# Optimization experiments

Hardware: AMD Instinct MI355X
Metric: run time of the kernel (lower is better)

The kernel has to match this reference:

```python
import jax, jax.numpy as jnp
import numpy as np

N_NODES = 20000
N_EDGES = 320000
DIMS = [256, 256, 128, 64]  # input_dim, hidden_dims...
EPS = 1e-5


def gcn_conv(x, w, b, src, dst, n):
    # PyG GCNConv: linear first, then symmetric-normalized aggregation with self-loops
    x = x @ w  # [N, out]
    loops = jnp.arange(n, dtype=src.dtype)
    src2 = jnp.concatenate([src, loops])
    dst2 = jnp.concatenate([dst, loops])
    deg = jax.ops.segment_sum(jnp.ones_like(dst2, dtype=x.dtype), dst2, num_segments=n)
    dinv = jnp.where(deg > 0, deg ** -0.5, 0.0)
    norm = dinv[src2] * dinv[dst2]  # [E+N]
    msg = x[src2] * norm[:, None]   # gathered, scaled messages
    out = jax.ops.segment_sum(msg, dst2, num_segments=n)
    return out + b


def graph_norm(x, w, b, a):
    # PyG GraphNorm over a single graph: per-feature mean/var across nodes
    mean = jnp.mean(x, axis=0)
    centered = x - a * mean
    var = jnp.mean(centered * centered, axis=0)
    return w * centered * jax.lax.rsqrt(var + EPS) + b


def layer_norm(x, w, b):
    mean = jnp.mean(x, axis=-1, keepdims=True)
    var = jnp.mean((x - mean) ** 2, axis=-1, keepdims=True)
    return (x - mean) * jax.lax.rsqrt(var + EPS) * w + b


def setup_inputs() -> dict:
    key = jax.random.key(0)
    ks = jax.random.split(key, 32)
    inp = {}
    inp["x"] = jax.random.normal(ks[0], (N_NODES, DIMS[0]), dtype=jnp.float32)
    inp["edge_index"] = jax.random.randint(ks[1], (2, N_EDGES), 0, N_NODES, dtype=jnp.int32)
    ki = 2
    for i in range(3):
        fin, fout = DIMS[i], DIMS[i + 1]
        s = 1.0 / np.sqrt(fin)
        inp[f"w{i}"] = jax.random.uniform(ks[ki], (fin, fout), jnp.float32, -s, s); ki += 1
        inp[f"b{i}"] = jnp.zeros((fout,), jnp.float32)
        inp[f"gn{i}_w"] = jnp.ones((fout,), jnp.float32)
        inp[f"gn{i}_b"] = jnp.zeros((fout,), jnp.float32)
        inp[f"gn{i}_a"] = jnp.ones((fout,), jnp.float32)
    h = DIMS[-1]
    s = 1.0 / np.sqrt(3 * h)
    inp["wc1"] = jax.random.uniform(ks[ki], (3 * h, h), jnp.float32, -s, s); ki += 1
    inp["bc1"] = jnp.zeros((h,), jnp.float32)
    inp["ln_w"] = jnp.ones((h,), jnp.float32)
    inp["ln_b"] = jnp.zeros((h,), jnp.float32)
    s = 1.0 / np.sqrt(h)
    inp["wc2"] = jax.random.uniform(ks[ki], (h, 2), jnp.float32, -s, s); ki += 1
    inp["bc2"] = jnp.zeros((2,), jnp.float32)
    return inp


def reference(x, edge_index,
              w0, b0, gn0_w, gn0_b, gn0_a,
              w1, b1, gn1_w, gn1_b, gn1_a,
              w2, b2, gn2_w, gn2_b, gn2_a,
              wc1, bc1, ln_w, ln_b, wc2, bc2):
    src, dst = edge_index[0], edge_index[1]
    n = x.shape[0]
    params = [(w0, b0, gn0_w, gn0_b, gn0_a),
              (w1, b1, gn1_w, gn1_b, gn1_a),
              (w2, b2, gn2_w, gn2_b, gn2_a)]
    for (w, b, gw, gb, ga) in params:
        x_res = x
        x = gcn_conv(x, w, b, src, dst, n)
        x = graph_norm(x, gw, gb, ga)
        x = jax.nn.gelu(x, approximate=False)
        # dropout = identity (eval); residual only when shapes match (layer 0)
        if x.shape == x_res.shape:
            x = x + x_res
    # multi-pool over the single graph (batch vector of zeros): mean | max | sum
    pooled = jnp.concatenate([jnp.mean(x, axis=0), jnp.max(x, axis=0), jnp.sum(x, axis=0)])[None, :]  # [1, 3h]
    h = pooled @ wc1 + bc1
    h = layer_norm(h, ln_w, ln_b)
    h = jax.nn.gelu(h, approximate=False)
    return h @ wc2 + bc2  # [1, num_classes]
```

## Files before the change

### kernel.cpp

```cpp
#include <hip/hip_runtime.h>
#include <math.h>

#define EPSV 1e-5f
#define MAXB 2176
#define GBLK 2080

typedef __attribute__((ext_vector_type(8))) short short8;
typedef __attribute__((ext_vector_type(4))) float f32x4;

__device__ __forceinline__ float gelu_f(float x) {
    return 0.5f * x * (1.0f + erff(x * 0.70710678118654752440f));
}

__device__ __forceinline__ float4 f4add(float4 a, float4 b) {
    return make_float4(a.x + b.x, a.y + b.y, a.z + b.z, a.w + b.w);
}

__device__ __forceinline__ ushort f2bf(float v) {
    union { float f; unsigned u; } a; a.f = v;
    unsigned r = a.u + 0x7FFFu + ((a.u >> 16) & 1u);
    return (ushort)(r >> 16);
}
__device__ __forceinline__ float bf2f(ushort h) {
    union { unsigned u; float f; } a; a.u = ((unsigned)h) << 16;
    return a.f;
}
__device__ __forceinline__ float4 bf4f(ushort4 v) {
    return make_float4(bf2f(v.x), bf2f(v.y), bf2f(v.z), bf2f(v.w));
}

__global__ void deg_kernel(const int* __restrict__ ei, int* __restrict__ deg, int E) {
    int stride = gridDim.x * blockDim.x;
    for (int e = blockIdx.x * blockDim.x + threadIdx.x; e < E; e += stride)
        atomicAdd(&deg[ei[E + e]], 1);
}

__global__ __launch_bounds__(1024) void scan_kernel(const int* __restrict__ deg,
                                                    int* __restrict__ off,
                                                    float* __restrict__ dinv, int N) {
    __shared__ int sh[1024];
    int t = threadIdx.x;
    int chunk = (N + 1023) >> 10;
    int b = t * chunk;
    int e = b + chunk; if (e > N) e = N;
    int s = 0;
    for (int i = b; i < e; ++i) s += deg[i];
    sh[t] = s;
    __syncthreads();
    for (int d = 1; d < 1024; d <<= 1) {
        int v = (t >= d) ? sh[t - d] : 0;
        __syncthreads();
        sh[t] += v;
        __syncthreads();
    }
    int run = (t > 0) ? sh[t - 1] : 0;
    for (int i = b; i < e; ++i) {
        off[i] = run;
        run += deg[i];
        dinv[i] = rsqrtf((float)(deg[i] + 1));
    }
    if (t == 1023) off[N] = sh[1023];
}

__global__ void fill_kernel(const int* __restrict__ ei, const int* __restrict__ off,
                            int* __restrict__ fill, int* __restrict__ csr, int E) {
    int stride = gridDim.x * blockDim.x;
    for (int e = blockIdx.x * blockDim.x + threadIdx.x; e < E; e += stride) {
        int d = ei[E + e];
        int p = off[d] + atomicAdd(&fill[d], 1);
        csr[p] = ei[e];
    }
}

__global__ __launch_bounds__(256) void packx_kernel(
    const float* __restrict__ x, ushort* __restrict__ hi, ushort* __restrict__ lo, long n)
{
    long stride = (long)gridDim.x * blockDim.x * 4;
    for (long i = ((long)blockIdx.x * blockDim.x + threadIdx.x) * 4; i < n; i += stride) {
        float4 v = *(const float4*)(x + i);
        ushort4 h, l2;
        h.x = f2bf(v.x); h.y = f2bf(v.y); h.z = f2bf(v.z); h.w = f2bf(v.w);
        l2.x = f2bf(v.x - bf2f(h.x)); l2.y = f2bf(v.y - bf2f(h.y));
        l2.z = f2bf(v.z - bf2f(h.z)); l2.w = f2bf(v.w - bf2f(h.w));
        *(ushort4*)(hi + i) = h;
        *(ushort4*)(lo + i) = l2;
    }
}

__global__ void packw_all_kernel(const float* __restrict__ w0, const float* __restrict__ w1,
                                 const float* __restrict__ w2,
                                 ushort* __restrict__ wthi, ushort* __restrict__ wtlo)
{
    int idx = blockIdx.x * 256 + threadIdx.x;
    const float* W; int K, F, base, local;
    if (idx < 65536)       { W = w0; K = 256; F = 256; base = 0;     local = idx; }
    else if (idx < 98304)  { W = w1; K = 256; F = 128; base = 65536; local = idx - 65536; }
    else if (idx < 106496) { W = w2; K = 128; F = 64;  base = 98304; local = idx - 98304; }
    else return;
    int k = local / F, f = local - k * F;
    float v = W[local];
    ushort h = f2bf(v);
    wthi[base + f * K + k] = h;
    wtlo[base + f * K + k] = f2bf(v - bf2f(h));
}

template<int K, int BN>
__global__ __launch_bounds__(256) void gemm_mfma_kernel(
    const ushort* __restrict__ ahi, const ushort* __restrict__ alo,
    const ushort* __restrict__ wthi, const ushort* __restrict__ wtlo,
    const float* __restrict__ dinv, ushort* __restrict__ C,
    int M, int F)
{
    constexpr int BM = 128, BK = 64;
    constexpr int LDK = BK + 8;
    constexpr int CF  = BN / 32;
    constexpr int WCH = BN / 32;

    __shared__ ushort AsH[BM * LDK], AsL[BM * LDK];
    __shared__ ushort WsH[BN * LDK], WsL[BN * LDK];

    const int tid = threadIdx.x;
    const int l = tid & 63, w = tid >> 6;
    const int wr = w >> 1, wc = w & 1;
    const int m0   = blockIdx.y * BM;
    const int colB = blockIdx.x * BN;
    const int lr = l & 15, lkg = l >> 4;

    f32x4 acc[4][CF] = {};

    for (int kk = 0; kk < K; kk += BK) {
        short8 ra[4], rb[4], rwh[WCH], rwl[WCH];
#pragma unroll
        for (int i = 0; i < 4; ++i) {
            int q = tid + i * 256;
            int row = q >> 3, cc = q & 7;
            int rg = m0 + row; if (rg > M - 1) rg = M - 1;
            ra[i] = *(const short8*)(ahi + (size_t)rg * K + kk + cc * 8);
            rb[i] = *(const short8*)(alo + (size_t)rg * K + kk + cc * 8);
        }
#pragma unroll
        for (int i = 0; i < WCH; ++i) {
            int q = tid + i * 256;
            int row = q >> 3, cc = q & 7;
            rwh[i] = *(const short8*)(wthi + (size_t)(colB + row) * K + kk + cc * 8);
            rwl[i] = *(const short8*)(wtlo + (size_t)(colB + row) * K + kk + cc * 8);
        }
        __syncthreads();
#pragma unroll
        for (int i = 0; i < 4; ++i) {
            int q = tid + i * 256;
            int row = q >> 3, cc = q & 7;
            *(short8*)&AsH[row * LDK + cc * 8] = ra[i];
            *(short8*)&AsL[row * LDK + cc * 8] = rb[i];
        }
#pragma unroll
        for (int i = 0; i < WCH; ++i) {
            int q = tid + i * 256;
            int row = q >> 3, cc = q & 7;
            *(short8*)&WsH[row * LDK + cc * 8] = rwh[i];
            *(short8*)&WsL[row * LDK + cc * 8] = rwl[i];
        }
        __syncthreads();

#pragma unroll
        for (int ks = 0; ks < 2; ++ks) {
            const int kof = ks * 32 + lkg * 8;
            short8 afh[4], afl[4];
#pragma unroll
            for (int rf = 0; rf < 4; ++rf) {
                int row = wr * 64 + rf * 16 + lr;
                afh[rf] = *(const short8*)&AsH[row * LDK + kof];
                afl[rf] = *(const short8*)&AsL[row * LDK + kof];
            }
            short8 wfh[CF], wfl[CF];
#pragma unroll
            for (int cf = 0; cf < CF; ++cf) {
                int row = wc * (BN / 2) + cf * 16 + lr;
                wfh[cf] = *(const short8*)&WsH[row * LDK + kof];
                wfl[cf] = *(const short8*)&WsL[row * LDK + kof];
            }
#pragma unroll
            for (int rf = 0; rf < 4; ++rf) {
#pragma unroll
                for (int cf = 0; cf < CF; ++cf) {
                    acc[rf][cf] = __builtin_amdgcn_mfma_f32_16x16x32_bf16(afh[rf], wfh[cf], acc[rf][cf], 0, 0, 0);
                    acc[rf][cf] = __builtin_amdgcn_mfma_f32_16x16x32_bf16(afh[rf], wfl[cf], acc[rf][cf], 0, 0, 0);
                    acc[rf][cf] = __builtin_amdgcn_mfma_f32_16x16x32_bf16(afl[rf], wfh[cf], acc[rf][cf], 0, 0, 0);
                }
            }
        }
    }

#pragma unroll
    for (int rf = 0; rf < 4; ++rf) {
#pragma unroll
        for (int j = 0; j < 4; ++j) {
            int r = m0 + wr * 64 + rf * 16 + lkg * 4 + j;
            if (r < M) {
                float dv = dinv[r];
                ushort* Cp = C + (size_t)r * F + colB + wc * (BN / 2) + lr;
#pragma unroll
                for (int cf = 0; cf < CF; ++cf)
                    Cp[cf * 16] = f2bf(acc[rf][cf][j] * dv);
            }
        }
    }
}

template<int F>
__global__ __launch_bounds__(256) void gather_kernel(
    const ushort* __restrict__ hs, const int* __restrict__ off,
    const int* __restrict__ csr, const float* __restrict__ dinv,
    const float* __restrict__ bias, float* __restrict__ t,
    float* __restrict__ p1, float* __restrict__ p2, int N)
{
    constexpr int NG  = F / 64;
    constexpr int LDR = F / 4;
    constexpr int NPB = 16;
    const int lane = threadIdx.x & 15;
    const int slot = threadIdx.x >> 4;

    const int xs    = blockIdx.x & 7;
    const int g     = xs % NG;
    const int r     = xs / NG;
    const int chunk = blockIdx.x >> 3;
    const int repl  = 8 / NG;
    const int nPerG = (int)(gridDim.x >> 3) * repl;
    const int j     = chunk * repl + r;

    const int col4 = g * 16 + lane;
    const int c0 = col4 * 4;
    float4* t4 = (float4*)t;
    const float4 bv = ((const float4*)bias)[col4];

    float4 a1 = make_float4(0.f, 0.f, 0.f, 0.f);
    float4 a2 = make_float4(0.f, 0.f, 0.f, 0.f);

    for (int d = j * NPB + slot; d < N; d += nPerG * NPB) {
        float4 acc = bf4f(*(const ushort4*)(hs + (size_t)d * F + c0));
        const int e0 = off[d], e1 = off[d + 1];
        int e = e0;
        for (; e + 8 <= e1; e += 8) {
            int s0 = csr[e + 0], s1 = csr[e + 1], s2 = csr[e + 2], s3 = csr[e + 3];
            int s4 = csr[e + 4], s5 = csr[e + 5], s6 = csr[e + 6], s7 = csr[e + 7];
            ushort4 v0 = *(const ushort4*)(hs + (size_t)s0 * F + c0);
            ushort4 v1 = *(const ushort4*)(hs + (size_t)s1 * F + c0);
            ushort4 v2 = *(const ushort4*)(hs + (size_t)s2 * F + c0);
            ushort4 v3 = *(const ushort4*)(hs + (size_t)s3 * F + c0);
            ushort4 v4 = *(const ushort4*)(hs + (size_t)s4 * F + c0);
            ushort4 v5 = *(const ushort4*)(hs + (size_t)s5 * F + c0);
            ushort4 v6 = *(const ushort4*)(hs + (size_t)s6 * F + c0);
            ushort4 v7 = *(const ushort4*)(hs + (size_t)s7 * F + c0);
            float4 u0 = f4add(bf4f(v0), bf4f(v1));
            float4 u1 = f4add(bf4f(v2), bf4f(v3));
            float4 u2 = f4add(bf4f(v4), bf4f(v5));
            float4 u3 = f4add(bf4f(v6), bf4f(v7));
            acc = f4add(acc, f4add(f4add(u0, u1), f4add(u2, u3)));
        }
        for (; e + 2 <= e1; e += 2) {
            int s0 = csr[e + 0], s1 = csr[e + 1];
            ushort4 v0 = *(const ushort4*)(hs + (size_t)s0 * F + c0);
            ushort4 v1 = *(const ushort4*)(hs + (size_t)s1 * F + c0);
            acc = f4add(acc, f4add(bf4f(v0), bf4f(v1)));
        }
        if (e < e1) {
            acc = f4add(acc, bf4f(*(const ushort4*)(hs + (size_t)csr[e] * F + c0)));
        }

        float dv = dinv[d];
        float4 o;
        o.x = fmaf(dv, acc.x, bv.x);
        o.y = fmaf(dv, acc.y, bv.y);
        o.z = fmaf(dv, acc.z, bv.z);
        o.w = fmaf(dv, acc.w, bv.w);
        t4[(long)d * LDR + col4] = o;
        a1.x += o.x; a1.y += o.y; a1.z += o.z; a1.w += o.w;
        a2.x += o.x * o.x; a2.y += o.y * o.y; a2.z += o.z * o.z; a2.w += o.w * o.w;
    }

    __shared__ float red[8][256];
    red[0][threadIdx.x] = a1.x; red[1][threadIdx.x] = a1.y;
    red[2][threadIdx.x] = a1.z; red[3][threadIdx.x] = a1.w;
    red[4][threadIdx.x] = a2.x; red[5][threadIdx.x] = a2.y;
    red[6][threadIdx.x] = a2.z; red[7][threadIdx.x] = a2.w;
    __syncthreads();
    if (slot == 0) {
        float sum[8];
#pragma unroll
        for (int k = 0; k < 8; ++k) {
            float s = red[k][lane];
            for (int jj = 1; jj < NPB; ++jj) s += red[k][jj * 16 + lane];
            sum[k] = s;
        }
        ((float4*)p1)[(long)col4 * MAXB + blockIdx.x] = make_float4(sum[0], sum[1], sum[2], sum[3]);
        ((float4*)p2)[(long)col4 * MAXB + blockIdx.x] = make_float4(sum[4], sum[5], sum[6], sum[7]);
    }
}

__global__ __launch_bounds__(256) void statreduce_kernel(
    const float* __restrict__ p1, const float* __restrict__ p2,
    const float* __restrict__ ga,
    float* __restrict__ meanv, float* __restrict__ istdv,
    int nb, int N, int NG)
{
    const int c4 = blockIdx.x;
    const int g = (c4 >> 4) % NG;
    const float4* p14 = (const float4*)p1 + (long)c4 * MAXB;
    const float4* p24 = (const float4*)p2 + (long)c4 * MAXB;
    float4 a1 = make_float4(0.f, 0.f, 0.f, 0.f);
    float4 a2 = make_float4(0.f, 0.f, 0.f, 0.f);
    for (int r = threadIdx.x; r < nb; r += 256) {
        if (((r & 7) % NG) != g) continue;
        float4 v1 = p14[r];
        float4 v2 = p24[r];
        a1.x += v1.x; a1.y += v1.y; a1.z += v1.z; a1.w += v1.w;
        a2.x += v2.x; a2.y += v2.y; a2.z += v2.z; a2.w += v2.w;
    }
#pragma unroll
    for (int offv = 32; offv > 0; offv >>= 1) {
        a1.x += __shfl_down(a1.x, offv); a1.y += __shfl_down(a1.y, offv);
        a1.z += __shfl_down(a1.z, offv); a1.w += __shfl_down(a1.w, offv);
        a2.x += __shfl_down(a2.x, offv); a2.y += __shfl_down(a2.y, offv);
        a2.z += __shfl_down(a2.z, offv); a2.w += __shfl_down(a2.w, offv);
    }
    __shared__ float4 sh1[4], sh2[4];
    const int wid = threadIdx.x >> 6;
    if ((threadIdx.x & 63) == 0) { sh1[wid] = a1; sh2[wid] = a2; }
    __syncthreads();
    if (threadIdx.x == 0) {
        float4 t1 = sh1[0], t2 = sh2[0];
        for (int jj = 1; jj < 4; ++jj) {
            float4 u1 = sh1[jj], u2 = sh2[jj];
            t1.x += u1.x; t1.y += u1.y; t1.z += u1.z; t1.w += u1.w;
            t2.x += u2.x; t2.y += u2.y; t2.z += u2.z; t2.w += u2.w;
        }
        float s1a[4] = { t1.x, t1.y, t1.z, t1.w };
        float s2a[4] = { t2.x, t2.y, t2.z, t2.w };
#pragma unroll
        for (int k = 0; k < 4; ++k) {
            int c = c4 * 4 + k;
            float m = s1a[k] / (float)N;
            float a = ga[c];
            float var = s2a[k] / (float)N - 2.f * a * m * m + a * a * m * m;
            meanv[c] = m;
            istdv[c] = rsqrtf(var + EPSV);
        }
    }
}

__global__ __launch_bounds__(256) void normgelu_kernel(
    const float* __restrict__ t, const float* __restrict__ meanv,
    const float* __restrict__ istdv, const float* __restrict__ gw,
    const float* __restrict__ gb, const float* __restrict__ ga,
    const float* __restrict__ res,
    ushort* __restrict__ ohi, ushort* __restrict__ olo,
    float* __restrict__ fpout,
    int log2f, long total)
{
    long stride = (long)gridDim.x * blockDim.x;
    int fmask = (1 << log2f) - 1;
    for (long idx = (long)blockIdx.x * blockDim.x + threadIdx.x; idx < total; idx += stride) {
        int c = (int)idx & fmask;
        float v = t[idx];
        float y = gw[c] * (v - ga[c] * meanv[c]) * istdv[c] + gb[c];
        y = gelu_f(y);
        if (res) y += res[idx];
        if (ohi) {
            ushort h = f2bf(y);
            ohi[idx] = h;
            olo[idx] = f2bf(y - bf2f(h));
        } else {
            fpout[idx] = y;
        }
    }
}

__device__ __forceinline__ void atomicMaxFloat(float* addr, float val) {
    unsigned* ua = (unsigned*)addr;
    unsigned old = *ua;
    while (true) {
        float of = __uint_as_float(old);
        if (of >= val) break;
        unsigned assumed = old;
        old = atomicCAS(ua, assumed, __float_as_uint(val));
        if (old == assumed) break;
    }
}

__global__ void initpool_kernel(float* __restrict__ psum, float* __restrict__ pmax) {
    int t = threadIdx.x;
    psum[t] = 0.f;
    pmax[t] = -INFINITY;
}

__global__ __launch_bounds__(256) void colpool_kernel(
    const float* __restrict__ x, float* __restrict__ psum, float* __restrict__ pmax,
    int M, int rowsPerBlock)
{
    int c = threadIdx.x & 63;
    int rl = threadIdx.x >> 6;
    int r0 = blockIdx.x * rowsPerBlock;
    int rend = r0 + rowsPerBlock; if (rend > M) rend = M;
    float a1 = 0.f, am = -INFINITY;
    for (int r = r0 + rl; r < rend; r += 4) {
        float v = x[(long)r * 64 + c];
        a1 += v; am = fmaxf(am, v);
    }
    __shared__ float sh1[256], shm[256];
    sh1[threadIdx.x] = a1; shm[threadIdx.x] = am;
    __syncthreads();
    if (threadIdx.x < 64) {
        for (int j = 1; j < 4; ++j) {
            a1 += sh1[c + j * 64];
            am = fmaxf(am, shm[c + j * 64]);
        }
        atomicAdd(&psum[c], a1);
        atomicMaxFloat(&pmax[c], am);
    }
}

__global__ void head_kernel(const float* __restrict__ psum, const float* __restrict__ pmax,
                            const float* __restrict__ wc1, const float* __restrict__ bc1,
                            const float* __restrict__ lnw, const float* __restrict__ lnb,
                            const float* __restrict__ wc2, const float* __restrict__ bc2,
                            float* __restrict__ out, int M)
{
    __shared__ float p[192];
    int t = threadIdx.x;
    float s = psum[t];
    p[t] = s / (float)M;
    p[64 + t] = pmax[t];
    p[128 + t] = s;
    __syncthreads();
    float h = bc1[t];
    for (int k = 0; k < 192; ++k) h = fmaf(p[k], wc1[k * 64 + t], h);
    float m = h;
    for (int off = 32; off > 0; off >>= 1) m += __shfl_xor(m, off);
    m *= (1.f / 64.f);
    float d = h - m;
    float v = d * d;
    for (int off = 32; off > 0; off >>= 1) v += __shfl_xor(v, off);
    v *= (1.f / 64.f);
    float y = d * rsqrtf(v + EPSV) * lnw[t] + lnb[t];
    y = gelu_f(y);
    float o0 = y * wc2[t * 2 + 0];
    float o1 = y * wc2[t * 2 + 1];
    for (int off = 32; off > 0; off >>= 1) {
        o0 += __shfl_xor(o0, off);
        o1 += __shfl_xor(o1, off);
    }
    if (t == 0) {
        out[0] = o0 + bc2[0];
        out[1] = o1 + bc2[1];
    }
}

extern "C" void kernel_launch(void* const* d_in, const int* in_sizes, int n_in,
                              void* d_out, int out_size, void* d_ws, size_t ws_size,
                              hipStream_t stream)
{
    const float* x    = (const float*)d_in[0];
    const int*   ei   = (const int*)d_in[1];
    const float* w0   = (const float*)d_in[2];
    const float* b0   = (const float*)d_in[3];
    const float* gn0w = (const float*)d_in[4];
    const float* gn0b = (const float*)d_in[5];
    const float* gn0a = (const float*)d_in[6];
    const float* w1   = (const float*)d_in[7];
    const float* b1   = (const float*)d_in[8];
    const float* gn1w = (const float*)d_in[9];
    const float* gn1b = (const float*)d_in[10];
    const float* gn1a = (const float*)d_in[11];
    const float* w2   = (const float*)d_in[12];
    const float* b2   = (const float*)d_in[13];
    const float* gn2w = (const float*)d_in[14];
    const float* gn2b = (const float*)d_in[15];
    const float* gn2a = (const float*)d_in[16];
    const float* wc1  = (const float*)d_in[17];
    const float* bc1  = (const float*)d_in[18];
    const float* lnw  = (const float*)d_in[19];
    const float* lnb  = (const float*)d_in[20];
    const float* wc2  = (const float*)d_in[21];
    const float* bc2  = (const float*)d_in[22];

    const int N = in_sizes[0] / 256;
    const int E = in_sizes[1] / 2;

    float* ws = (float*)d_ws;
    const size_t BIG = (size_t)N * 256;
    float* B0    = ws;
    float* B1    = ws + BIG;
    float* dinv  = ws + 2 * BIG;
    int*   deg   = (int*)(dinv + N);
    int*   fill  = deg + N;
    int*   off   = fill + N;
    int*   csr   = off + N + 1;
    float* p1    = (float*)(csr + E);
    float* p2    = p1 + (size_t)64 * MAXB * 4;
    float* meanv = p2 + (size_t)64 * MAXB * 4;
    float* istdv = meanv + 256;
    float* psum  = istdv + 256;
    float* pmax  = psum + 64;
    ushort* wthi = (ushort*)(pmax + 64);
    ushort* wtlo = wthi + 106496;
    const int woff[3] = { 0, 65536, 98304 };

    hipMemsetAsync(deg, 0, (size_t)2 * N * sizeof(int), stream);
    deg_kernel<<<1024, 256, 0, stream>>>(ei, deg, E);
    scan_kernel<<<1, 1024, 0, stream>>>(deg, off, dinv, N);
    fill_kernel<<<1024, 256, 0, stream>>>(ei, off, fill, csr, E);

    packw_all_kernel<<<416, 256, 0, stream>>>(w0, w1, w2, wthi, wtlo);
    packx_kernel<<<1280, 256, 0, stream>>>(x, (ushort*)B0, (ushort*)B0 + BIG, (long)BIG);

    struct Layer {
        const float *b, *gw, *gb, *ga;
        int K, F, lf;
    } L[3] = {
        { b0, gn0w, gn0b, gn0a, 256, 256, 8 },
        { b1, gn1w, gn1b, gn1a, 256, 128, 7 },
        { b2, gn2w, gn2b, gn2a, 128,  64, 6 },
    };
    const float* resb[3] = { x, nullptr, nullptr };
    float* Bb[2] = { B0, B1 };

    int cur = 0;
    for (int li = 0; li < 3; ++li) {
        const int K = L[li].K, F = L[li].F, lf = L[li].lf;
        const long total = (long)N << lf;
        float* Ab = Bb[cur];
        float* HSf = Bb[cur ^ 1];
        ushort* ahi = (ushort*)Ab;
        ushort* alo = ahi + BIG;
        ushort* HS = (ushort*)HSf;

        const int rowTiles = (N + 127) / 128;
        if (li == 0) {
            gemm_mfma_kernel<256, 128><<<dim3(2, rowTiles), 256, 0, stream>>>(
                ahi, alo, wthi + woff[0], wtlo + woff[0], dinv, HS, N, F);
        } else if (li == 1) {
            gemm_mfma_kernel<256, 128><<<dim3(1, rowTiles), 256, 0, stream>>>(
                ahi, alo, wthi + woff[1], wtlo + woff[1], dinv, HS, N, F);
        } else {
            gemm_mfma_kernel<128, 64><<<dim3(1, rowTiles), 256, 0, stream>>>(
                ahi, alo, wthi + woff[2], wtlo + woff[2], dinv, HS, N, F);
        }

        float* T = Ab;
        if (F == 256)
            gather_kernel<256><<<GBLK, 256, 0, stream>>>(HS, off, csr, dinv, L[li].b, T, p1, p2, N);
        else if (F == 128)
            gather_kernel<128><<<GBLK, 256, 0, stream>>>(HS, off, csr, dinv, L[li].b, T, p1, p2, N);
        else
            gather_kernel<64><<<GBLK, 256, 0, stream>>>(HS, off, csr, dinv, L[li].b, T, p1, p2, N);

        statreduce_kernel<<<F / 4, 256, 0, stream>>>(p1, p2, L[li].ga, meanv, istdv, GBLK, N, F / 64);

        long fb = (total + 255) / 256; if (fb > 4096) fb = 4096;
        ushort* ohi = (li < 2) ? (ushort*)HSf : nullptr;
        ushort* olo = (li < 2) ? (ushort*)HSf + BIG : nullptr;
        float*  fpo = (li == 2) ? HSf : nullptr;
        normgelu_kernel<<<(int)fb, 256, 0, stream>>>(T, meanv, istdv,
                                                     L[li].gw, L[li].gb, L[li].ga,
                                                     resb[li], ohi, olo, fpo, lf, total);
        cur ^= 1;
    }

    initpool_kernel<<<1, 64, 0, stream>>>(psum, pmax);
    colpool_kernel<<<(N + 127) / 128, 256, 0, stream>>>(Bb[cur], psum, pmax, N, 128);
    head_kernel<<<1, 64, 0, stream>>>(psum, pmax, wc1, bc1, lnw, lnb, wc2, bc2,
                                      (float*)d_out, N);
}
```

Measured before the change: 280.0 us.

## Fuse small kernels via last-block reductions and convert input inside GEMM

Folds the degree scan into the degree-count kernel, the per-feature stat reduction into the gather kernel, and pooling plus the classifier head into one kernel. Each uses an atomic counter so the last finishing block does the final reduction. The separate pass that splits x into bf16 hi/lo is removed, and the layer-0 GEMM now does that split on the fp32 input as it loads it. The norm+GELU kernel is vectorised to float4. This cuts kernel launches and one full pass over x, but the final reductions now run on a single block, which serialises that step.

Result: slower. 1.060 ms (+278.6%).

```diff
diff --git a/kernel.cpp b/kernel.cpp
--- a/kernel.cpp
+++ b/kernel.cpp
@@ -28,26 +28,44 @@
 __device__ __forceinline__ float4 bf4f(ushort4 v) {
     return make_float4(bf2f(v.x), bf2f(v.y), bf2f(v.z), bf2f(v.w));
 }
-
-__global__ void deg_kernel(const int* __restrict__ ei, int* __restrict__ deg, int E) {
+__device__ __forceinline__ void f8_to_bf(const float4 f0, const float4 f1,
+                                         short8& h, short8& l) {
+    union { short8 v; ushort u[8]; } H, L;
+    float f[8] = { f0.x, f0.y, f0.z, f0.w, f1.x, f1.y, f1.z, f1.w };
+#pragma unroll
+    for (int j = 0; j < 8; ++j) {
+        H.u[j] = f2bf(f[j]);
+        L.u[j] = f2bf(f[j] - bf2f(H.u[j]));
+    }
+    h = H.v; l = L.v;
+}
+
+__global__ __launch_bounds__(256) void deg_scan_kernel(
+    const int* __restrict__ ei, int* __restrict__ deg,
+    int* __restrict__ off, float* __restrict__ dinv,
+    int E, int N, int* __restrict__ ctr)
+{
     int stride = gridDim.x * blockDim.x;
     for (int e = blockIdx.x * blockDim.x + threadIdx.x; e < E; e += stride)
         atomicAdd(&deg[ei[E + e]], 1);
-}
-
-__global__ __launch_bounds__(1024) void scan_kernel(const int* __restrict__ deg,
-                                                    int* __restrict__ off,
-                                                    float* __restrict__ dinv, int N) {
-    __shared__ int sh[1024];
-    int t = threadIdx.x;
-    int chunk = (N + 1023) >> 10;
+    __threadfence();
+    __shared__ int lastBlk;
+    if (threadIdx.x == 0)
+        lastBlk = (atomicAdd(ctr, 1) == (int)gridDim.x - 1);
+    __syncthreads();
+    if (!lastBlk) return;
+    __threadfence();
+
+    __shared__ int sh[256];
+    const int t = threadIdx.x;
+    const int chunk = (N + 255) >> 8;
     int b = t * chunk;
     int e = b + chunk; if (e > N) e = N;
     int s = 0;
     for (int i = b; i < e; ++i) s += deg[i];
     sh[t] = s;
     __syncthreads();
-    for (int d = 1; d < 1024; d <<= 1) {
+    for (int d = 1; d < 256; d <<= 1) {
         int v = (t >= d) ? sh[t - d] : 0;
         __syncthreads();
         sh[t] += v;
@@ -55,11 +73,12 @@
     }
     int run = (t > 0) ? sh[t - 1] : 0;
     for (int i = b; i < e; ++i) {
+        int dg = deg[i];
         off[i] = run;
-        run += deg[i];
-        dinv[i] = rsqrtf((float)(deg[i] + 1));
-    }
-    if (t == 1023) off[N] = sh[1023];
+        dinv[i] = rsqrtf((float)(dg + 1));
+        run += dg;
+    }
+    if (t == 255) off[N] = sh[255];
 }
 
 __global__ void fill_kernel(const int* __restrict__ ei, const int* __restrict__ off,
@@ -69,21 +88,6 @@
         int d = ei[E + e];
         int p = off[d] + atomicAdd(&fill[d], 1);
         csr[p] = ei[e];
-    }
-}
-
-__global__ __launch_bounds__(256) void packx_kernel(
-    const float* __restrict__ x, ushort* __restrict__ hi, ushort* __restrict__ lo, long n)
-{
-    long stride = (long)gridDim.x * blockDim.x * 4;
-    for (long i = ((long)blockIdx.x * blockDim.x + threadIdx.x) * 4; i < n; i += stride) {
-        float4 v = *(const float4*)(x + i);
-        ushort4 h, l2;
-        h.x = f2bf(v.x); h.y = f2bf(v.y); h.z = f2bf(v.z); h.w = f2bf(v.w);
-        l2.x = f2bf(v.x - bf2f(h.x)); l2.y = f2bf(v.y - bf2f(h.y));
-        l2.z = f2bf(v.z - bf2f(h.z)); l2.w = f2bf(v.w - bf2f(h.w));
-        *(ushort4*)(hi + i) = h;
-        *(ushort4*)(lo + i) = l2;
     }
 }
 
@@ -104,9 +108,10 @@
     wtlo[base + f * K + k] = f2bf(v - bf2f(h));
 }
 
-template<int K, int BN>
+template<int K, int BN, bool AF32>
 __global__ __launch_bounds__(256) void gemm_mfma_kernel(
     const ushort* __restrict__ ahi, const ushort* __restrict__ alo,
+    const float* __restrict__ axf,
     const ushort* __restrict__ wthi, const ushort* __restrict__ wtlo,
     const float* __restrict__ dinv, ushort* __restrict__ C,
     int M, int F)
@@ -135,8 +140,13 @@
             int q = tid + i * 256;
             int row = q >> 3, cc = q & 7;
             int rg = m0 + row; if (rg > M - 1) rg = M - 1;
-            ra[i] = *(const short8*)(ahi + (size_t)rg * K + kk + cc * 8);
-            rb[i] = *(const short8*)(alo + (size_t)rg * K + kk + cc * 8);
+            if constexpr (AF32) {
+                const float* xp = axf + (size_t)rg * K + kk + cc * 8;
+                f8_to_bf(*(const float4*)xp, *(const float4*)(xp + 4), ra[i], rb[i]);
+            } else {
+                ra[i] = *(const short8*)(ahi + (size_t)rg * K + kk + cc * 8);
+                rb[i] = *(const short8*)(alo + (size_t)rg * K + kk + cc * 8);
+            }
         }
 #pragma unroll
         for (int i = 0; i < WCH; ++i) {
@@ -212,7 +222,10 @@
     const ushort* __restrict__ hs, const int* __restrict__ off,
     const int* __restrict__ csr, const float* __restrict__ dinv,
     const float* __restrict__ bias, float* __restrict__ t,
-    float* __restrict__ p1, float* __restrict__ p2, int N)
+    float* __restrict__ p1, float* __restrict__ p2,
+    const float* __restrict__ ga,
+    float* __restrict__ meanv, float* __restrict__ istdv,
+    int N, int* __restrict__ ctr)
 {
     constexpr int NG  = F / 64;
     constexpr int LDR = F / 4;
@@ -288,57 +301,53 @@
         float sum[8];
 #pragma unroll
         for (int k = 0; k < 8; ++k) {
-            float s = red[k][lane];
-            for (int jj = 1; jj < NPB; ++jj) s += red[k][jj * 16 + lane];
+            float s = red[k][threadIdx.x];
+            for (int jj = 1; jj < NPB; ++jj) s += red[k][jj * 16 + threadIdx.x];
             sum[k] = s;
         }
         ((float4*)p1)[(long)col4 * MAXB + blockIdx.x] = make_float4(sum[0], sum[1], sum[2], sum[3]);
         ((float4*)p2)[(long)col4 * MAXB + blockIdx.x] = make_float4(sum[4], sum[5], sum[6], sum[7]);
     }
-}
-
-__global__ __launch_bounds__(256) void statreduce_kernel(
-    const float* __restrict__ p1, const float* __restrict__ p2,
-    const float* __restrict__ ga,
-    float* __restrict__ meanv, float* __restrict__ istdv,
-    int nb, int N, int NG)
-{
-    const int c4 = blockIdx.x;
-    const int g = (c4 >> 4) % NG;
-    const float4* p14 = (const float4*)p1 + (long)c4 * MAXB;
-    const float4* p24 = (const float4*)p2 + (long)c4 * MAXB;
-    float4 a1 = make_float4(0.f, 0.f, 0.f, 0.f);
-    float4 a2 = make_float4(0.f, 0.f, 0.f, 0.f);
-    for (int r = threadIdx.x; r < nb; r += 256) {
-        if (((r & 7) % NG) != g) continue;
-        float4 v1 = p14[r];
-        float4 v2 = p24[r];
-        a1.x += v1.x; a1.y += v1.y; a1.z += v1.z; a1.w += v1.w;
-        a2.x += v2.x; a2.y += v2.y; a2.z += v2.z; a2.w += v2.w;
-    }
-#pragma unroll
-    for (int offv = 32; offv > 0; offv >>= 1) {
-        a1.x += __shfl_down(a1.x, offv); a1.y += __shfl_down(a1.y, offv);
-        a1.z += __shfl_down(a1.z, offv); a1.w += __shfl_down(a1.w, offv);
-        a2.x += __shfl_down(a2.x, offv); a2.y += __shfl_down(a2.y, offv);
-        a2.z += __shfl_down(a2.z, offv); a2.w += __shfl_down(a2.w, offv);
-    }
-    __shared__ float4 sh1[4], sh2[4];
-    const int wid = threadIdx.x >> 6;
-    if ((threadIdx.x & 63) == 0) { sh1[wid] = a1; sh2[wid] = a2; }
-    __syncthreads();
-    if (threadIdx.x == 0) {
-        float4 t1 = sh1[0], t2 = sh2[0];
-        for (int jj = 1; jj < 4; ++jj) {
-            float4 u1 = sh1[jj], u2 = sh2[jj];
-            t1.x += u1.x; t1.y += u1.y; t1.z += u1.z; t1.w += u1.w;
-            t2.x += u2.x; t2.y += u2.y; t2.z += u2.z; t2.w += u2.w;
-        }
-        float s1a[4] = { t1.x, t1.y, t1.z, t1.w };
-        float s2a[4] = { t2.x, t2.y, t2.z, t2.w };
+
+    __threadfence();
+    __shared__ int lastBlk;
+    if (threadIdx.x == 0)
+        lastBlk = (atomicAdd(ctr, 1) == (int)gridDim.x - 1);
+    __syncthreads();
+    if (!lastBlk) return;
+    __threadfence();
+
+    constexpr int C4   = F / 4;
+    constexpr int NSUB = 256 / C4;
+    const int c4r = threadIdx.x & (C4 - 1);
+    const int sub = threadIdx.x / C4;
+    const int gr  = (c4r >> 4) % NG;
+    const float4* p14 = (const float4*)p1 + (long)c4r * MAXB;
+    const float4* p24 = (const float4*)p2 + (long)c4r * MAXB;
+    const int nbq = (int)(gridDim.x >> 3);
+
+    float4 s1 = make_float4(0.f, 0.f, 0.f, 0.f);
+    float4 s2 = make_float4(0.f, 0.f, 0.f, 0.f);
+    for (int q = sub; q < nbq; q += NSUB) {
+        for (int s = gr; s < 8; s += NG) {
+            int rr = q * 8 + s;
+            s1 = f4add(s1, p14[rr]);
+            s2 = f4add(s2, p24[rr]);
+        }
+    }
+    __shared__ float4 sr1[256], sr2[256];
+    sr1[threadIdx.x] = s1; sr2[threadIdx.x] = s2;
+    __syncthreads();
+    if (sub == 0) {
+        for (int jj = 1; jj < NSUB; ++jj) {
+            s1 = f4add(s1, sr1[c4r + jj * C4]);
+            s2 = f4add(s2, sr2[c4r + jj * C4]);
+        }
+        float s1a[4] = { s1.x, s1.y, s1.z, s1.w };
+        float s2a[4] = { s2.x, s2.y, s2.z, s2.w };
 #pragma unroll
         for (int k = 0; k < 4; ++k) {
-            int c = c4 * 4 + k;
+            int c = c4r * 4 + k;
             float m = s1a[k] / (float)N;
             float a = ga[c];
             float var = s2a[k] / (float)N - 2.f * a * m * m + a * a * m * m;
@@ -355,52 +364,50 @@
     const float* __restrict__ res,
     ushort* __restrict__ ohi, ushort* __restrict__ olo,
     float* __restrict__ fpout,
-    int log2f, long total)
+    int fmask4, long total4)
 {
     long stride = (long)gridDim.x * blockDim.x;
-    int fmask = (1 << log2f) - 1;
-    for (long idx = (long)blockIdx.x * blockDim.x + threadIdx.x; idx < total; idx += stride) {
-        int c = (int)idx & fmask;
-        float v = t[idx];
-        float y = gw[c] * (v - ga[c] * meanv[c]) * istdv[c] + gb[c];
-        y = gelu_f(y);
-        if (res) y += res[idx];
+    const float4* t4 = (const float4*)t;
+    for (long i4 = (long)blockIdx.x * blockDim.x + threadIdx.x; i4 < total4; i4 += stride) {
+        int c4 = (int)i4 & fmask4;
+        float4 v = t4[i4];
+        float4 mv = ((const float4*)meanv)[c4];
+        float4 iv = ((const float4*)istdv)[c4];
+        float4 gwv = ((const float4*)gw)[c4];
+        float4 gbv = ((const float4*)gb)[c4];
+        float4 gav = ((const float4*)ga)[c4];
+        float y0 = gelu_f(gwv.x * (v.x - gav.x * mv.x) * iv.x + gbv.x);
+        float y1 = gelu_f(gwv.y * (v.y - gav.y * mv.y) * iv.y + gbv.y);
+        float y2 = gelu_f(gwv.z * (v.z - gav.z * mv.z) * iv.z + gbv.z);
+        float y3 = gelu_f(gwv.w * (v.w - gav.w * mv.w) * iv.w + gbv.w);
+        if (res) {
+            float4 rv = ((const float4*)res)[i4];
+            y0 += rv.x; y1 += rv.y; y2 += rv.z; y3 += rv.w;
+        }
         if (ohi) {
-            ushort h = f2bf(y);
-            ohi[idx] = h;
-            olo[idx] = f2bf(y - bf2f(h));
+            ushort4 h, lo4;
+            h.x = f2bf(y0); h.y = f2bf(y1); h.z = f2bf(y2); h.w = f2bf(y3);
+            lo4.x = f2bf(y0 - bf2f(h.x)); lo4.y = f2bf(y1 - bf2f(h.y));
+            lo4.z = f2bf(y2 - bf2f(h.z)); lo4.w = f2bf(y3 - bf2f(h.w));
+            ((ushort4*)ohi)[i4] = h;
+            ((ushort4*)olo)[i4] = lo4;
         } else {
-            fpout[idx] = y;
-        }
-    }
-}
-
-__device__ __forceinline__ void atomicMaxFloat(float* addr, float val) {
-    unsigned* ua = (unsigned*)addr;
-    unsigned old = *ua;
-    while (true) {
-        float of = __uint_as_float(old);
-        if (of >= val) break;
-        unsigned assumed = old;
-        old = atomicCAS(ua, assumed, __float_as_uint(val));
-        if (old == assumed) break;
-    }
-}
-
-__global__ void initpool_kernel(float* __restrict__ psum, float* __restrict__ pmax) {
-    int t = threadIdx.x;
-    psum[t] = 0.f;
-    pmax[t] = -INFINITY;
-}
-
-__global__ __launch_bounds__(256) void colpool_kernel(
-    const float* __restrict__ x, float* __restrict__ psum, float* __restrict__ pmax,
-    int M, int rowsPerBlock)
-{
-    int c = threadIdx.x & 63;
-    int rl = threadIdx.x >> 6;
-    int r0 = blockIdx.x * rowsPerBlock;
-    int rend = r0 + rowsPerBlock; if (rend > M) rend = M;
+            ((float4*)fpout)[i4] = make_float4(y0, y1, y2, y3);
+        }
+    }
+}
+
+__global__ __launch_bounds__(256) void pool_head_kernel(
+    const float* __restrict__ x, float* __restrict__ pp1, float* __restrict__ ppm,
+    int M,
+    const float* __restrict__ wc1, const float* __restrict__ bc1,
+    const float* __restrict__ lnw, const float* __restrict__ lnb,
+    const float* __restrict__ wc2, const float* __restrict__ bc2,
+    float* __restrict__ out, int* __restrict__ ctr)
+{
+    const int c = threadIdx.x & 63, rl = threadIdx.x >> 6;
+    int r0 = blockIdx.x * 128;
+    int rend = r0 + 128; if (rend > M) rend = M;
     float a1 = 0.f, am = -INFINITY;
     for (int r = r0 + rl; r < rend; r += 4) {
         float v = x[(long)r * 64 + c];
@@ -414,44 +421,59 @@
             a1 += sh1[c + j * 64];
             am = fmaxf(am, shm[c + j * 64]);
         }
-        atomicAdd(&psum[c], a1);
-        atomicMaxFloat(&pmax[c], am);
-    }
-}
-
-__global__ void head_kernel(const float* __restrict__ psum, const float* __restrict__ pmax,
-                            const float* __restrict__ wc1, const float* __restrict__ bc1,
-                            const float* __restrict__ lnw, const float* __restrict__ lnb,
-                            const float* __restrict__ wc2, const float* __restrict__ bc2,
-                            float* __restrict__ out, int M)
-{
+        pp1[blockIdx.x * 64 + c] = a1;
+        ppm[blockIdx.x * 64 + c] = am;
+    }
+    __threadfence();
+    __shared__ int lastBlk;
+    if (threadIdx.x == 0)
+        lastBlk = (atomicAdd(ctr, 1) == (int)gridDim.x - 1);
+    __syncthreads();
+    if (!lastBlk) return;
+    __threadfence();
+
+    float s = 0.f, mx = -INFINITY;
+    for (int r = rl; r < (int)gridDim.x; r += 4) {
+        s += pp1[r * 64 + c];
+        mx = fmaxf(mx, ppm[r * 64 + c]);
+    }
+    __syncthreads();
+    sh1[threadIdx.x] = s; shm[threadIdx.x] = mx;
+    __syncthreads();
     __shared__ float p[192];
-    int t = threadIdx.x;
-    float s = psum[t];
-    p[t] = s / (float)M;
-    p[64 + t] = pmax[t];
-    p[128 + t] = s;
-    __syncthreads();
-    float h = bc1[t];
-    for (int k = 0; k < 192; ++k) h = fmaf(p[k], wc1[k * 64 + t], h);
-    float m = h;
-    for (int off = 32; off > 0; off >>= 1) m += __shfl_xor(m, off);
-    m *= (1.f / 64.f);
-    float d = h - m;
-    float v = d * d;
-    for (int off = 32; off > 0; off >>= 1) v += __shfl_xor(v, off);
-    v *= (1.f / 64.f);
-    float y = d * rsqrtf(v + EPSV) * lnw[t] + lnb[t];
-    y = gelu_f(y);
-    float o0 = y * wc2[t * 2 + 0];
-    float o1 = y * wc2[t * 2 + 1];
-    for (int off = 32; off > 0; off >>= 1) {
-        o0 += __shfl_xor(o0, off);
-        o1 += __shfl_xor(o1, off);
-    }
-    if (t == 0) {
-        out[0] = o0 + bc2[0];
-        out[1] = o1 + bc2[1];
+    if (threadIdx.x < 64) {
+        for (int j = 1; j < 4; ++j) {
+            s += sh1[c + j * 64];
+            mx = fmaxf(mx, shm[c + j * 64]);
+        }
+        p[c] = s / (float)M;
+        p[64 + c] = mx;
+        p[128 + c] = s;
+    }
+    __syncthreads();
+    if (threadIdx.x < 64) {
+        int t = threadIdx.x;
+        float h = bc1[t];
+        for (int k = 0; k < 192; ++k) h = fmaf(p[k], wc1[k * 64 + t], h);
+        float m = h;
+        for (int o = 32; o > 0; o >>= 1) m += __shfl_xor(m, o);
+        m *= (1.f / 64.f);
+        float d = h - m;
+        float v = d * d;
+        for (int o = 32; o > 0; o >>= 1) v += __shfl_xor(v, o);
+        v *= (1.f / 64.f);
+        float y = d * rsqrtf(v + EPSV) * lnw[t] + lnb[t];
+        y = gelu_f(y);
+        float o0 = y * wc2[t * 2 + 0];
+        float o1 = y * wc2[t * 2 + 1];
+        for (int o = 32; o > 0; o >>= 1) {
+            o0 += __shfl_xor(o0, o);
+            o1 += __shfl_xor(o1, o);
+        }
+        if (t == 0) {
+            out[0] = o0 + bc2[0];
+            out[1] = o1 + bc2[1];
+        }
     }
 }
 
@@ -493,25 +515,23 @@
     float* dinv  = ws + 2 * BIG;
     int*   deg   = (int*)(dinv + N);
     int*   fill  = deg + N;
-    int*   off   = fill + N;
+    int*   ctrs  = fill + N;
+    int*   off   = ctrs + 8;
     int*   csr   = off + N + 1;
     float* p1    = (float*)(csr + E);
     float* p2    = p1 + (size_t)64 * MAXB * 4;
     float* meanv = p2 + (size_t)64 * MAXB * 4;
     float* istdv = meanv + 256;
-    float* psum  = istdv + 256;
-    float* pmax  = psum + 64;
-    ushort* wthi = (ushort*)(pmax + 64);
+    float* pp1   = istdv + 256;
+    float* ppm   = pp1 + 16384;
+    ushort* wthi = (ushort*)(ppm + 16384);
     ushort* wtlo = wthi + 106496;
     const int woff[3] = { 0, 65536, 98304 };
 
-    hipMemsetAsync(deg, 0, (size_t)2 * N * sizeof(int), stream);
-    deg_kernel<<<1024, 256, 0, stream>>>(ei, deg, E);
-    scan_kernel<<<1, 1024, 0, stream>>>(deg, off, dinv, N);
+    hipMemsetAsync(deg, 0, ((size_t)2 * N + 8) * sizeof(int), stream);
+    deg_scan_kernel<<<1024, 256, 0, stream>>>(ei, deg, off, dinv, E, N, ctrs + 0);
     fill_kernel<<<1024, 256, 0, stream>>>(ei, off, fill, csr, E);
-
     packw_all_kernel<<<416, 256, 0, stream>>>(w0, w1, w2, wthi, wtlo);
-    packx_kernel<<<1280, 256, 0, stream>>>(x, (ushort*)B0, (ushort*)B0 + BIG, (long)BIG);
 
     struct Layer {
         const float *b, *gw, *gb, *ga;
@@ -536,38 +556,40 @@
 
         const int rowTiles = (N + 127) / 128;
         if (li == 0) {
-            gemm_mfma_kernel<256, 128><<<dim3(2, rowTiles), 256, 0, stream>>>(
-                ahi, alo, wthi + woff[0], wtlo + woff[0], dinv, HS, N, F);
+            gemm_mfma_kernel<256, 128, true><<<dim3(2, rowTiles), 256, 0, stream>>>(
+                nullptr, nullptr, x, wthi + woff[0], wtlo + woff[0], dinv, HS, N, F);
         } else if (li == 1) {
-            gemm_mfma_kernel<256, 128><<<dim3(1, rowTiles), 256, 0, stream>>>(
-                ahi, alo, wthi + woff[1], wtlo + woff[1], dinv, HS, N, F);
+            gemm_mfma_kernel<256, 128, false><<<dim3(1, rowTiles), 256, 0, stream>>>(
+                ahi, alo, nullptr, wthi + woff[1], wtlo + woff[1], dinv, HS, N, F);
         } else {
-            gemm_mfma_kernel<128, 64><<<dim3(1, rowTiles), 256, 0, stream>>>(
-                ahi, alo, wthi + woff[2], wtlo + woff[2], dinv, HS, N, F);
+            gemm_mfma_kernel<128, 64, false><<<dim3(1, rowTiles), 256, 0, stream>>>(
+                ahi, alo, nullptr, wthi + woff[2], wtlo + woff[2], dinv, HS, N, F);
         }
 
         float* T = Ab;
         if (F == 256)
-            gather_kernel<256><<<GBLK, 256, 0, stream>>>(HS, off, csr, dinv, L[li].b, T, p1, p2, N);
+            gather_kernel<256><<<GBLK, 256, 0, stream>>>(HS, off, csr, dinv, L[li].b, T,
+                p1, p2, L[li].ga, meanv, istdv, N, ctrs + 1 + li);
         else if (F == 128)
-            gather_kernel<128><<<GBLK, 256, 0, stream>>>(HS, off, csr, dinv, L[li].b, T, p1, p2, N);
+            gather_kernel<128><<<GBLK, 256, 0, stream>>>(HS, off, csr, dinv, L[li].b, T,
+                p1, p2, L[li].ga, meanv, istdv, N, ctrs + 1 + li);
         else
-            gather_kernel<64><<<GBLK, 256, 0, stream>>>(HS, off, csr, dinv, L[li].b, T, p1, p2, N);
-
-        statreduce_kernel<<<F / 4, 256, 0, stream>>>(p1, p2, L[li].ga, meanv, istdv, GBLK, N, F / 64);
-
-        long fb = (total + 255) / 256; if (fb > 4096) fb = 4096;
+            gather_kernel<64><<<GBLK, 256, 0, stream>>>(HS, off, csr, dinv, L[li].b, T,
+                p1, p2, L[li].ga, meanv, istdv, N, ctrs + 1 + li);
+
+        long total4 = total >> 2;
+        long fb = (total4 + 255) / 256; if (fb > 2048) fb = 2048;
         ushort* ohi = (li < 2) ? (ushort*)HSf : nullptr;
         ushort* olo = (li < 2) ? (ushort*)HSf + BIG : nullptr;
         float*  fpo = (li == 2) ? HSf : nullptr;
         normgelu_kernel<<<(int)fb, 256, 0, stream>>>(T, meanv, istdv,
                                                      L[li].gw, L[li].gb, L[li].ga,
-                                                     resb[li], ohi, olo, fpo, lf, total);
+                                                     resb[li], ohi, olo, fpo,
+                                                     (1 << (lf - 2)) - 1, total4);
         cur ^= 1;
     }
 
-    initpool_kernel<<<1, 64, 0, stream>>>(psum, pmax);
-    colpool_kernel<<<(N + 127) / 128, 256, 0, stream>>>(Bb[cur], psum, pmax, N, 128);
-    head_kernel<<<1, 64, 0, stream>>>(psum, pmax, wc1, bc1, lnw, lnb, wc2, bc2,
-                                      (float*)d_out, N);
-}
+    pool_head_kernel<<<(N + 127) / 128, 256, 0, stream>>>(
+        Bb[cur], pp1, ppm, N, wc1, bc1, lnw, lnb, wc2, bc2,
+        (float*)d_out, ctrs + 4);
+}
```

## Fuse GraphNorm+GELU+residual into next GEMM's A-load and pooling; store aggregates in bf16

Applied to the files above, without the earlier changes.

Removes the standalone normgelu and packx kernels. The GEMM now loads fp32 x (layer 0), or loads the bf16 gather output and applies GraphNorm, GELU and the residual on the fly before splitting into hi/lo bf16. The final layer's norm and GELU are applied inside the column-pooling kernel. Gather outputs are stored as bf16 instead of fp32, which cuts memory traffic but adds rounding error. GELU is recomputed once per column block for layer 0's output, since layer 1's GEMM grid has one column tile.

Result: no change. 275.0 us (-1.8%).

```diff
diff --git a/kernel.cpp b/kernel.cpp
--- a/kernel.cpp
+++ b/kernel.cpp
@@ -27,6 +27,15 @@
 }
 __device__ __forceinline__ float4 bf4f(ushort4 v) {
     return make_float4(bf2f(v.x), bf2f(v.y), bf2f(v.z), bf2f(v.w));
+}
+__device__ __forceinline__ void f8_to_bf(const float* f, short8& h, short8& l) {
+    union { short8 v; ushort u[8]; } H, L;
+#pragma unroll
+    for (int j = 0; j < 8; ++j) {
+        H.u[j] = f2bf(f[j]);
+        L.u[j] = f2bf(f[j] - bf2f(H.u[j]));
+    }
+    h = H.v; l = L.v;
 }
 
 __global__ void deg_kernel(const int* __restrict__ ei, int* __restrict__ deg, int E) {
@@ -72,21 +81,6 @@
     }
 }
 
-__global__ __launch_bounds__(256) void packx_kernel(
-    const float* __restrict__ x, ushort* __restrict__ hi, ushort* __restrict__ lo, long n)
-{
-    long stride = (long)gridDim.x * blockDim.x * 4;
-    for (long i = ((long)blockIdx.x * blockDim.x + threadIdx.x) * 4; i < n; i += stride) {
-        float4 v = *(const float4*)(x + i);
-        ushort4 h, l2;
-        h.x = f2bf(v.x); h.y = f2bf(v.y); h.z = f2bf(v.z); h.w = f2bf(v.w);
-        l2.x = f2bf(v.x - bf2f(h.x)); l2.y = f2bf(v.y - bf2f(h.y));
-        l2.z = f2bf(v.z - bf2f(h.z)); l2.w = f2bf(v.w - bf2f(h.w));
-        *(ushort4*)(hi + i) = h;
-        *(ushort4*)(lo + i) = l2;
-    }
-}
-
 __global__ void packw_all_kernel(const float* __restrict__ w0, const float* __restrict__ w1,
                                  const float* __restrict__ w2,
                                  ushort* __restrict__ wthi, ushort* __restrict__ wtlo)
@@ -104,9 +98,13 @@
     wtlo[base + f * K + k] = f2bf(v - bf2f(h));
 }
 
-template<int K, int BN>
+template<int K, int BN, int MODE>
 __global__ __launch_bounds__(256) void gemm_mfma_kernel(
-    const ushort* __restrict__ ahi, const ushort* __restrict__ alo,
+    const float* __restrict__ axf,
+    const ushort* __restrict__ tsrc,
+    const float* __restrict__ tm, const float* __restrict__ tis,
+    const float* __restrict__ tgw, const float* __restrict__ tgb,
+    const float* __restrict__ tga, const float* __restrict__ res,
     const ushort* __restrict__ wthi, const ushort* __restrict__ wtlo,
     const float* __restrict__ dinv, ushort* __restrict__ C,
     int M, int F)
@@ -135,8 +133,38 @@
             int q = tid + i * 256;
             int row = q >> 3, cc = q & 7;
             int rg = m0 + row; if (rg > M - 1) rg = M - 1;
-            ra[i] = *(const short8*)(ahi + (size_t)rg * K + kk + cc * 8);
-            rb[i] = *(const short8*)(alo + (size_t)rg * K + kk + cc * 8);
+            int kc = kk + cc * 8;
+            float y[8];
+            if constexpr (MODE == 0) {
+                const float* xp = axf + (size_t)rg * K + kc;
+                float4 v0 = *(const float4*)xp, v1 = *(const float4*)(xp + 4);
+                y[0]=v0.x; y[1]=v0.y; y[2]=v0.z; y[3]=v0.w;
+                y[4]=v1.x; y[5]=v1.y; y[6]=v1.z; y[7]=v1.w;
+            } else {
+                const ushort* tp = tsrc + (size_t)rg * K + kc;
+                float4 v0 = bf4f(*(const ushort4*)tp);
+                float4 v1 = bf4f(*(const ushort4*)(tp + 4));
+                float4 m0v = *(const float4*)(tm + kc),  m1v = *(const float4*)(tm + kc + 4);
+                float4 i0v = *(const float4*)(tis + kc), i1v = *(const float4*)(tis + kc + 4);
+                float4 w0v = *(const float4*)(tgw + kc), w1v = *(const float4*)(tgw + kc + 4);
+                float4 b0v = *(const float4*)(tgb + kc), b1v = *(const float4*)(tgb + kc + 4);
+                float4 a0v = *(const float4*)(tga + kc), a1v = *(const float4*)(tga + kc + 4);
+                y[0] = gelu_f(w0v.x * (v0.x - a0v.x * m0v.x) * i0v.x + b0v.x);
+                y[1] = gelu_f(w0v.y * (v0.y - a0v.y * m0v.y) * i0v.y + b0v.y);
+                y[2] = gelu_f(w0v.z * (v0.z - a0v.z * m0v.z) * i0v.z + b0v.z);
+                y[3] = gelu_f(w0v.w * (v0.w - a0v.w * m0v.w) * i0v.w + b0v.w);
+                y[4] = gelu_f(w1v.x * (v1.x - a1v.x * m1v.x) * i1v.x + b1v.x);
+                y[5] = gelu_f(w1v.y * (v1.y - a1v.y * m1v.y) * i1v.y + b1v.y);
+                y[6] = gelu_f(w1v.z * (v1.z - a1v.z * m1v.z) * i1v.z + b1v.z);
+                y[7] = gelu_f(w1v.w * (v1.w - a1v.w * m1v.w) * i1v.w + b1v.w);
+                if (res) {
+                    const float* rp = res + (size_t)rg * K + kc;
+                    float4 r0 = *(const float4*)rp, r1 = *(const float4*)(rp + 4);
+                    y[0] += r0.x; y[1] += r0.y; y[2] += r0.z; y[3] += r0.w;
+                    y[4] += r1.x; y[5] += r1.y; y[6] += r1.z; y[7] += r1.w;
+                }
+            }
+            f8_to_bf(y, ra[i], rb[i]);
         }
 #pragma unroll
         for (int i = 0; i < WCH; ++i) {
@@ -211,11 +239,10 @@
 __global__ __launch_bounds__(256) void gather_kernel(
     const ushort* __restrict__ hs, const int* __restrict__ off,
     const int* __restrict__ csr, const float* __restrict__ dinv,
-    const float* __restrict__ bias, float* __restrict__ t,
+    const float* __restrict__ bias, ushort* __restrict__ t,
     float* __restrict__ p1, float* __restrict__ p2, int N)
 {
     constexpr int NG  = F / 64;
-    constexpr int LDR = F / 4;
     constexpr int NPB = 16;
     const int lane = threadIdx.x & 15;
     const int slot = threadIdx.x >> 4;
@@ -230,7 +257,6 @@
 
     const int col4 = g * 16 + lane;
     const int c0 = col4 * 4;
-    float4* t4 = (float4*)t;
     const float4 bv = ((const float4*)bias)[col4];
 
     float4 a1 = make_float4(0.f, 0.f, 0.f, 0.f);
@@ -273,7 +299,9 @@
         o.y = fmaf(dv, acc.y, bv.y);
         o.z = fmaf(dv, acc.z, bv.z);
         o.w = fmaf(dv, acc.w, bv.w);
-        t4[(long)d * LDR + col4] = o;
+        ushort4 ov;
+        ov.x = f2bf(o.x); ov.y = f2bf(o.y); ov.z = f2bf(o.z); ov.w = f2bf(o.w);
+        *(ushort4*)(t + (size_t)d * F + c0) = ov;
         a1.x += o.x; a1.y += o.y; a1.z += o.z; a1.w += o.w;
         a2.x += o.x * o.x; a2.y += o.y * o.y; a2.z += o.z * o.z; a2.w += o.w * o.w;
     }
@@ -348,33 +376,6 @@
     }
 }
 
-__global__ __launch_bounds__(256) void normgelu_kernel(
-    const float* __restrict__ t, const float* __restrict__ meanv,
-    const float* __restrict__ istdv, const float* __restrict__ gw,
-    const float* __restrict__ gb, const float* __restrict__ ga,
-    const float* __restrict__ res,
-    ushort* __restrict__ ohi, ushort* __restrict__ olo,
-    float* __restrict__ fpout,
-    int log2f, long total)
-{
-    long stride = (long)gridDim.x * blockDim.x;
-    int fmask = (1 << log2f) - 1;
-    for (long idx = (long)blockIdx.x * blockDim.x + threadIdx.x; idx < total; idx += stride) {
-        int c = (int)idx & fmask;
-        float v = t[idx];
-        float y = gw[c] * (v - ga[c] * meanv[c]) * istdv[c] + gb[c];
-        y = gelu_f(y);
-        if (res) y += res[idx];
-        if (ohi) {
-            ushort h = f2bf(y);
-            ohi[idx] = h;
-            olo[idx] = f2bf(y - bf2f(h));
-        } else {
-            fpout[idx] = y;
-        }
-    }
-}
-
 __device__ __forceinline__ void atomicMaxFloat(float* addr, float val) {
     unsigned* ua = (unsigned*)addr;
     unsigned old = *ua;
@@ -393,18 +394,23 @@
     pmax[t] = -INFINITY;
 }
 
-__global__ __launch_bounds__(256) void colpool_kernel(
-    const float* __restrict__ x, float* __restrict__ psum, float* __restrict__ pmax,
+__global__ __launch_bounds__(256) void colpool_ng_kernel(
+    const ushort* __restrict__ t, const float* __restrict__ meanv,
+    const float* __restrict__ istdv, const float* __restrict__ gw,
+    const float* __restrict__ gb, const float* __restrict__ ga,
+    float* __restrict__ psum, float* __restrict__ pmax,
     int M, int rowsPerBlock)
 {
     int c = threadIdx.x & 63;
     int rl = threadIdx.x >> 6;
     int r0 = blockIdx.x * rowsPerBlock;
     int rend = r0 + rowsPerBlock; if (rend > M) rend = M;
+    const float mc = meanv[c], ic = istdv[c], wc_ = gw[c], bc_ = gb[c], ac = ga[c];
     float a1 = 0.f, am = -INFINITY;
     for (int r = r0 + rl; r < rend; r += 4) {
-        float v = x[(long)r * 64 + c];
-        a1 += v; am = fmaxf(am, v);
+        float v = bf2f(t[(long)r * 64 + c]);
+        float y = gelu_f(wc_ * (v - ac * mc) * ic + bc_);
+        a1 += y; am = fmaxf(am, y);
     }
     __shared__ float sh1[256], shm[256];
     sh1[threadIdx.x] = a1; shm[threadIdx.x] = am;
@@ -488,8 +494,8 @@
 
     float* ws = (float*)d_ws;
     const size_t BIG = (size_t)N * 256;
-    float* B0    = ws;
-    float* B1    = ws + BIG;
+    ushort* HS   = (ushort*)ws;
+    ushort* T    = (ushort*)(ws + BIG);
     float* dinv  = ws + 2 * BIG;
     int*   deg   = (int*)(dinv + N);
     int*   fill  = deg + N;
@@ -509,65 +515,40 @@
     deg_kernel<<<1024, 256, 0, stream>>>(ei, deg, E);
     scan_kernel<<<1, 1024, 0, stream>>>(deg, off, dinv, N);
     fill_kernel<<<1024, 256, 0, stream>>>(ei, off, fill, csr, E);
-
     packw_all_kernel<<<416, 256, 0, stream>>>(w0, w1, w2, wthi, wtlo);
-    packx_kernel<<<1280, 256, 0, stream>>>(x, (ushort*)B0, (ushort*)B0 + BIG, (long)BIG);
 
     struct Layer {
         const float *b, *gw, *gb, *ga;
-        int K, F, lf;
+        int K, F;
     } L[3] = {
-        { b0, gn0w, gn0b, gn0a, 256, 256, 8 },
-        { b1, gn1w, gn1b, gn1a, 256, 128, 7 },
-        { b2, gn2w, gn2b, gn2a, 128,  64, 6 },
+        { b0, gn0w, gn0b, gn0a, 256, 256 },
+        { b1, gn1w, gn1b, gn1a, 256, 128 },
+        { b2, gn2w, gn2b, gn2a, 128,  64 },
     };
-    const float* resb[3] = { x, nullptr, nullptr };
-    float* Bb[2] = { B0, B1 };
-
-    int cur = 0;
-    for (int li = 0; li < 3; ++li) {
-        const int K = L[li].K, F = L[li].F, lf = L[li].lf;
-        const long total = (long)N << lf;
-        float* Ab = Bb[cur];
-        float* HSf = Bb[cur ^ 1];
-        ushort* ahi = (ushort*)Ab;
-        ushort* alo = ahi + BIG;
-        ushort* HS = (ushort*)HSf;
-
-        const int rowTiles = (N + 127) / 128;
-        if (li == 0) {
-            gemm_mfma_kernel<256, 128><<<dim3(2, rowTiles), 256, 0, stream>>>(
-                ahi, alo, wthi + woff[0], wtlo + woff[0], dinv, HS, N, F);
-        } else if (li == 1) {
-            gemm_mfma_kernel<256, 128><<<dim3(1, rowTiles), 256, 0, stream>>>(
-                ahi, alo, wthi + woff[1], wtlo + woff[1], dinv, HS, N, F);
-        } else {
-            gemm_mfma_kernel<128, 64><<<dim3(1, rowTiles), 256, 0, stream>>>(
-                ahi, alo, wthi + woff[2], wtlo + woff[2], dinv, HS, N, F);
-        }
-
-        float* T = Ab;
-        if (F == 256)
-            gather_kernel<256><<<GBLK, 256, 0, stream>>>(HS, off, csr, dinv, L[li].b, T, p1, p2, N);
-        else if (F == 128)
-            gather_kernel<128><<<GBLK, 256, 0, stream>>>(HS, off, csr, dinv, L[li].b, T, p1, p2, N);
-        else
-            gather_kernel<64><<<GBLK, 256, 0, stream>>>(HS, off, csr, dinv, L[li].b, T, p1, p2, N);
-
-        statreduce_kernel<<<F / 4, 256, 0, stream>>>(p1, p2, L[li].ga, meanv, istdv, GBLK, N, F / 64);
-
-        long fb = (total + 255) / 256; if (fb > 4096) fb = 4096;
-        ushort* ohi = (li < 2) ? (ushort*)HSf : nullptr;
-        ushort* olo = (li < 2) ? (ushort*)HSf + BIG : nullptr;
-        float*  fpo = (li == 2) ? HSf : nullptr;
-        normgelu_kernel<<<(int)fb, 256, 0, stream>>>(T, meanv, istdv,
-                                                     L[li].gw, L[li].gb, L[li].ga,
-                                                     resb[li], ohi, olo, fpo, lf, total);
-        cur ^= 1;
-    }
+
+    const int rowTiles = (N + 127) / 128;
+
+    gemm_mfma_kernel<256, 128, 0><<<dim3(2, rowTiles), 256, 0, stream>>>(
+        x, nullptr, nullptr, nullptr, nullptr, nullptr, nullptr, nullptr,
+        wthi + woff[0], wtlo + woff[0], dinv, HS, N, 256);
+    gather_kernel<256><<<GBLK, 256, 0, stream>>>(HS, off, csr, dinv, L[0].b, T, p1, p2, N);
+    statreduce_kernel<<<64, 256, 0, stream>>>(p1, p2, L[0].ga, meanv, istdv, GBLK, N, 4);
+
+    gemm_mfma_kernel<256, 128, 1><<<dim3(1, rowTiles), 256, 0, stream>>>(
+        nullptr, T, meanv, istdv, L[0].gw, L[0].gb, L[0].ga, x,
+        wthi + woff[1], wtlo + woff[1], dinv, HS, N, 128);
+    gather_kernel<128><<<GBLK, 256, 0, stream>>>(HS, off, csr, dinv, L[1].b, T, p1, p2, N);
+    statreduce_kernel<<<32, 256, 0, stream>>>(p1, p2, L[1].ga, meanv, istdv, GBLK, N, 2);
+
+    gemm_mfma_kernel<128, 64, 1><<<dim3(1, rowTiles), 256, 0, stream>>>(
+        nullptr, T, meanv, istdv, L[1].gw, L[1].gb, L[1].ga, nullptr,
+        wthi + woff[2], wtlo + woff[2], dinv, HS, N, 64);
+    gather_kernel<64><<<GBLK, 256, 0, stream>>>(HS, off, csr, dinv, L[2].b, T, p1, p2, N);
+    statreduce_kernel<<<16, 256, 0, stream>>>(p1, p2, L[2].ga, meanv, istdv, GBLK, N, 1);
 
     initpool_kernel<<<1, 64, 0, stream>>>(psum, pmax);
-    colpool_kernel<<<(N + 127) / 128, 256, 0, stream>>>(Bb[cur], psum, pmax, N, 128);
+    colpool_ng_kernel<<<(N + 127) / 128, 256, 0, stream>>>(
+        T, meanv, istdv, L[2].gw, L[2].gb, L[2].ga, psum, pmax, N, 128);
     head_kernel<<<1, 64, 0, stream>>>(psum, pmax, wc1, bc1, lnw, lnb, wc2, bc2,
                                       (float*)d_out, N);
 }
```
